# Kernel optimization log

Measured on AMD Instinct MI355X. Metric: run time of the kernel, lower is better.

Reference implementation:

```python
import jax, jax.numpy as jnp
import numpy as np

N = 100000   # n_nodes
E = 800000   # n_edges
IN = 128
HID = 128
OUT = 40
EPS = 1e-5   # BatchNorm1d eps


def setup_inputs() -> dict:
    key = jax.random.key(0)
    ks = jax.random.split(key, 16)
    def w(k, i, o):
        return jax.random.normal(k, (i, o), jnp.float32) / np.sqrt(i).astype(np.float32)
    return {
        "x": jax.random.normal(ks[0], (N, IN), jnp.float32),
        "edge_index": jax.random.randint(ks[1], (2, E), 0, N, dtype=jnp.int64),
        # SAGEConv weights: Wl acts on aggregated neighbors, Wr on root features
        "Wl0": w(ks[2], IN, HID),  "Wr0": w(ks[3], IN, HID),
        "Wl1": w(ks[4], HID, HID), "Wr1": w(ks[5], HID, HID),
        "Wl2": w(ks[6], HID, OUT), "Wr2": w(ks[7], HID, OUT),
        "b2": jnp.zeros((OUT,), jnp.float32),  # bias only on last layer
        # BatchNorm params for layers 0,1 (last layer has no BN)
        "g0": jnp.ones((HID,), jnp.float32), "be0": jnp.zeros((HID,), jnp.float32),
        "g1": jnp.ones((HID,), jnp.float32), "be1": jnp.zeros((HID,), jnp.float32),
    }


def _sage_conv(x, src, dst, Wl, Wr, b=None):
    # mean aggregation of source messages at destination nodes
    msg = x[src]                                             # [E, d] gather
    agg = jax.ops.segment_sum(msg, dst, num_segments=N)      # [N, d]
    cnt = jax.ops.segment_sum(jnp.ones((src.shape[0],), x.dtype), dst,
                              num_segments=N)                # [N]
    mean = agg / jnp.maximum(cnt, 1.0)[:, None]
    out = mean @ Wl + x @ Wr
    if b is not None:
        out = out + b
    return out


def _batch_norm(h, gamma, beta):
    # training-mode BN over node dim, biased variance (matches torch BatchNorm1d)
    mu = h.mean(axis=0)
    var = h.var(axis=0)
    return (h - mu) * jax.lax.rsqrt(var + EPS) * gamma + beta


def reference(x, edge_index, Wl0, Wr0, Wl1, Wr1, Wl2, Wr2, b2, g0, be0, g1, be1):
    src, dst = edge_index[0], edge_index[1]
    h = _sage_conv(x, src, dst, Wl0, Wr0)
    h = jax.nn.relu(_batch_norm(h, g0, be0))
    h = _sage_conv(h, src, dst, Wl1, Wr1)
    h = jax.nn.relu(_batch_norm(h, g1, be1))
    h = _sage_conv(h, src, dst, Wl2, Wr2, b2)
    return h
```

## Files before the change

kernel.cpp:

```cpp
#include <hip/hip_runtime.h>
#include <hip/hip_bf16.h>

#define N_NODES 100000
#define N_EDGES 800000
#define EPS 1e-5f
#define NBANK 32
#define HB_BLOCKS 256
#define HB_PER 3125
#define CS_GPB 64
#define BUCKET_N 12500
#define MROW 68

typedef __attribute__((ext_vector_type(8))) short short8;
typedef __attribute__((ext_vector_type(4))) float floatx4;

__device__ __forceinline__ unsigned short f2b(float f) {
    unsigned int u = __float_as_uint(f);
    u = (u + 0x7fffu + ((u >> 16) & 1u)) >> 16;
    return (unsigned short)u;
}
__device__ __forceinline__ float blo(unsigned int u) { return __uint_as_float(u << 16); }
__device__ __forceinline__ float bhi(unsigned int u) { return __uint_as_float(u & 0xffff0000u); }
__device__ __forceinline__ float b2f(unsigned short s) {
    return __uint_as_float(((unsigned int)s) << 16);
}

__global__ void __launch_bounds__(256) prep_k(const float* __restrict__ x,
                                              unsigned short* __restrict__ o,
                                              const int* __restrict__ dst,
                                              unsigned int* __restrict__ cnt,
                                              unsigned int* __restrict__ bhist) {
    if (blockIdx.x < 12500) {
        int i = blockIdx.x * 256 + threadIdx.x;
        float4 v = ((const float4*)x)[i];
        ushort4 r;
        r.x = f2b(v.x); r.y = f2b(v.y); r.z = f2b(v.z); r.w = f2b(v.w);
        ((ushort4*)o)[i] = r;
        return;
    }
    __shared__ unsigned int lh[8];
    int hb = blockIdx.x - 12500;
    if (threadIdx.x < 8) lh[threadIdx.x] = 0;
    __syncthreads();
    int start = hb * HB_PER;
    for (int i = threadIdx.x; i < HB_PER; i += 256) {
        int d = dst[start + i];
        atomicAdd(&cnt[d], 1u);
        atomicAdd(&lh[(unsigned int)d / BUCKET_N], 1u);
    }
    __syncthreads();
    if (threadIdx.x < 8) bhist[threadIdx.x * HB_BLOCKS + hb] = lh[threadIdx.x];
}

__device__ __forceinline__ void pack_one(const float* __restrict__ Wl,
                                         const float* __restrict__ Wr,
                                         unsigned short* __restrict__ out,
                                         int Hreal, int NCT, int tid) {
    int i = tid & 7;
    int lane = (tid >> 3) & 63;
    int q = tid >> 9;
    int c = q % NCT;
    int t = q / NCT;
    int k = t * 32 + (lane >> 4) * 8 + i;
    int n = c * 16 + (lane & 15);
    float v = 0.f;
    if (n < Hreal) v = (k < 128) ? Wl[k * Hreal + n] : Wr[(k - 128) * Hreal + n];
    out[tid] = f2b(v);
}

__global__ void __launch_bounds__(256) pack_all(const float* __restrict__ Wl0, const float* __restrict__ Wr0,
                                                const float* __restrict__ Wl1, const float* __restrict__ Wr1,
                                                const float* __restrict__ Wl2, const float* __restrict__ Wr2,
                                                unsigned short* __restrict__ W0p,
                                                unsigned short* __restrict__ W1p,
                                                unsigned short* __restrict__ W2p) {
    int tid = blockIdx.x * 256 + threadIdx.x;
    if (tid < 32768) pack_one(Wl0, Wr0, W0p, 128, 8, tid);
    else if (tid < 65536) pack_one(Wl1, Wr1, W1p, 128, 8, tid - 32768);
    else if (tid < 77824) pack_one(Wl2, Wr2, W2p, 40, 3, tid - 65536);
}

__global__ void scan1(const unsigned int* __restrict__ cnt, unsigned int* __restrict__ rowptr,
                      unsigned int* __restrict__ bsum) {
    __shared__ unsigned int sh[256];
    int t = threadIdx.x;
    int i = blockIdx.x * 256 + t;
    unsigned int v = (i < N_NODES) ? cnt[i] : 0u;
    sh[t] = v; __syncthreads();
    for (int off = 1; off < 256; off <<= 1) {
        unsigned int add = (t >= off) ? sh[t - off] : 0u;
        __syncthreads();
        sh[t] += add;
        __syncthreads();
    }
    if (i < N_NODES) rowptr[i] = sh[t] - v;
    if (t == 255) bsum[blockIdx.x] = sh[255];
}

__global__ void scan2_bscan(const unsigned int* __restrict__ bsum, unsigned int* __restrict__ boff,
                            int nb, unsigned int* __restrict__ A) {
    if (blockIdx.x == 0) {
        __shared__ unsigned int sh[512];
        int t = threadIdx.x;
        unsigned int v = (t < nb) ? bsum[t] : 0u;
        sh[t] = v; __syncthreads();
        for (int off = 1; off < 512; off <<= 1) {
            unsigned int add = (t >= off) ? sh[t - off] : 0u;
            __syncthreads();
            sh[t] += add;
            __syncthreads();
        }
        if (t < nb) boff[t] = sh[t] - v;
        return;
    }
    __shared__ unsigned int part[256];
    int t = threadIdx.x;
    unsigned int v[8];
    unsigned int s = 0;
    if (t < 256) {
#pragma unroll
        for (int i = 0; i < 8; i++) { v[i] = A[t * 8 + i]; s += v[i]; }
        part[t] = s;
    }
    __syncthreads();
    for (int off = 1; off < 256; off <<= 1) {
        unsigned int add = (t < 256 && t >= off) ? part[t - off] : 0u;
        __syncthreads();
        if (t < 256) part[t] += add;
        __syncthreads();
    }
    if (t < 256) {
        unsigned int base = part[t] - s;
#pragma unroll
        for (int i = 0; i < 8; i++) { unsigned int old = v[i]; A[t * 8 + i] = base; base += old; }
    }
}

__global__ void __launch_bounds__(256) scan3_bscatter(unsigned int* __restrict__ rowptr,
                                                      const unsigned int* __restrict__ boff,
                                                      unsigned int* __restrict__ cursor,
                                                      const int* __restrict__ src,
                                                      const int* __restrict__ dst,
                                                      const unsigned int* __restrict__ boffs,
                                                      unsigned int* __restrict__ ebuf) {
    if (blockIdx.x < 391) {
        int i = blockIdx.x * 256 + threadIdx.x;
        if (i < N_NODES) {
            unsigned int r = rowptr[i] + boff[blockIdx.x];
            rowptr[i] = r;
            cursor[i] = r;
        }
        if (i == N_NODES) rowptr[N_NODES] = N_EDGES;
        return;
    }
    __shared__ unsigned int cur[8];
    int bb = blockIdx.x - 391;
    if (threadIdx.x < 8) cur[threadIdx.x] = boffs[threadIdx.x * HB_BLOCKS + bb];
    __syncthreads();
    int start = bb * HB_PER;
    for (int i = threadIdx.x; i < HB_PER; i += 256) {
        int d = dst[start + i];
        int s = src[start + i];
        unsigned int b = (unsigned int)d / BUCKET_N;
        unsigned int dl = (unsigned int)d - b * BUCKET_N;
        unsigned int pos = atomicAdd(&cur[b], 1u);
        ebuf[pos] = (unsigned int)s | (dl << 17);
    }
}

__global__ void __launch_bounds__(256) cscatter(const unsigned int* __restrict__ ebuf,
                                                const unsigned int* __restrict__ rowptr,
                                                unsigned int* __restrict__ cursor,
                                                int* __restrict__ srclist) {
    int g = blockIdx.x & 7;
    int gblk = blockIdx.x >> 3;
    unsigned int estart = rowptr[g * BUCKET_N];
    unsigned int eend = (g == 7) ? N_EDGES : rowptr[(g + 1) * BUCKET_N];
    unsigned int nume = eend - estart;
    unsigned int per = (nume + CS_GPB - 1) / CS_GPB;
    unsigned int s0 = estart + gblk * per;
    unsigned int s1 = s0 + per; if (s1 > eend) s1 = eend;
    unsigned int nodebase = g * BUCKET_N;
    for (unsigned int i = s0 + threadIdx.x; i < s1; i += 256) {
        unsigned int p = ebuf[i];
        unsigned int s = p & 0x1FFFFu;
        unsigned int node = nodebase + (p >> 17);
        unsigned int pos = atomicAdd(&cursor[node], 1u);
        srclist[pos] = (int)s;
    }
}

template<int BN>
__device__ __forceinline__ void agg_phase16(const unsigned short* __restrict__ hb,
                                            const unsigned int* __restrict__ rowptr,
                                            const int* __restrict__ srclist,
                                            unsigned int* __restrict__ smean,
                                            const float* __restrict__ sc,
                                            const float* __restrict__ sh,
                                            int wave, int g, int l, int blockrow) {
    const uint4* hp = (const uint4*)hb;
    int nl = wave * 4 + g;
    int node = blockrow + nl;
    float f0 = 0.f, f1 = 0.f, f2 = 0.f, f3 = 0.f, f4 = 0.f, f5 = 0.f, f6 = 0.f, f7 = 0.f;
    float sc0r = 0.f, sc1r = 0.f, sc2r = 0.f, sc3r = 0.f, sc4r = 0.f, sc5r = 0.f, sc6r = 0.f, sc7r = 0.f;
    float sh0r = 0.f, sh1r = 0.f, sh2r = 0.f, sh3r = 0.f, sh4r = 0.f, sh5r = 0.f, sh6r = 0.f, sh7r = 0.f;
    if (BN) {
        const float* s0 = sc + l * 8;
        const float* s1 = sh + l * 8;
        sc0r = s0[0]; sc1r = s0[1]; sc2r = s0[2]; sc3r = s0[3];
        sc4r = s0[4]; sc5r = s0[5]; sc6r = s0[6]; sc7r = s0[7];
        sh0r = s1[0]; sh1r = s1[1]; sh2r = s1[2]; sh3r = s1[3];
        sh4r = s1[4]; sh5r = s1[5]; sh6r = s1[6]; sh7r = s1[7];
    }
    unsigned int b = rowptr[node], e = rowptr[node + 1];
    unsigned int p = b;
#define ACC8(U) { \
    if (BN) { \
        f0 += fmaxf(0.f, fmaf(blo(U.x), sc0r, sh0r)); \
        f1 += fmaxf(0.f, fmaf(bhi(U.x), sc1r, sh1r)); \
        f2 += fmaxf(0.f, fmaf(blo(U.y), sc2r, sh2r)); \
        f3 += fmaxf(0.f, fmaf(bhi(U.y), sc3r, sh3r)); \
        f4 += fmaxf(0.f, fmaf(blo(U.z), sc4r, sh4r)); \
        f5 += fmaxf(0.f, fmaf(bhi(U.z), sc5r, sh5r)); \
        f6 += fmaxf(0.f, fmaf(blo(U.w), sc6r, sh6r)); \
        f7 += fmaxf(0.f, fmaf(bhi(U.w), sc7r, sh7r)); \
    } else { \
        f0 += blo(U.x); f1 += bhi(U.x); f2 += blo(U.y); f3 += bhi(U.y); \
        f4 += blo(U.z); f5 += bhi(U.z); f6 += blo(U.w); f7 += bhi(U.w); \
    } }
    int s0 = 0, s1 = 0, s2 = 0, s3 = 0;
    bool have = (p + 4 <= e);
    if (have) { s0 = srclist[p]; s1 = srclist[p + 1]; s2 = srclist[p + 2]; s3 = srclist[p + 3]; }
    while (have) {
        uint4 u0 = hp[(size_t)s0 * 16 + l];
        uint4 u1 = hp[(size_t)s1 * 16 + l];
        uint4 u2 = hp[(size_t)s2 * 16 + l];
        uint4 u3 = hp[(size_t)s3 * 16 + l];
        p += 4;
        have = (p + 4 <= e);
        if (have) { s0 = srclist[p]; s1 = srclist[p + 1]; s2 = srclist[p + 2]; s3 = srclist[p + 3]; }
        ACC8(u0); ACC8(u1); ACC8(u2); ACC8(u3);
    }
    if (p + 2 <= e) {
        int t0 = srclist[p];
        int t1 = srclist[p + 1];
        uint4 u0 = hp[(size_t)t0 * 16 + l];
        uint4 u1 = hp[(size_t)t1 * 16 + l];
        ACC8(u0); ACC8(u1);
        p += 2;
    }
    if (p < e) {
        int t0 = srclist[p];
        uint4 u0 = hp[(size_t)t0 * 16 + l];
        ACC8(u0);
    }
#undef ACC8
    unsigned int deg = e - b;
    float r = 1.0f / (float)(deg > 1u ? deg : 1u);
    uint4 o;
    o.x = (unsigned int)f2b(f0 * r) | ((unsigned int)f2b(f1 * r) << 16);
    o.y = (unsigned int)f2b(f2 * r) | ((unsigned int)f2b(f3 * r) << 16);
    o.z = (unsigned int)f2b(f4 * r) | ((unsigned int)f2b(f5 * r) << 16);
    o.w = (unsigned int)f2b(f6 * r) | ((unsigned int)f2b(f7 * r) << 16);
    *(uint4*)&smean[nl * MROW + l * 4] = o;
}

__device__ __forceinline__ short8 bn_pack8(short8 raw, const float* __restrict__ scb,
                                           const float* __restrict__ shb, int koff) {
    short8 r;
#pragma unroll
    for (int i = 0; i < 8; i++) {
        float v = b2f((unsigned short)raw[i]);
        v = fmaxf(0.f, fmaf(v, scb[koff + i], shb[koff + i]));
        r[i] = (short)f2b(v);
    }
    return r;
}

template<int BN>
__global__ void __launch_bounds__(256) gemm2f_k(const unsigned short* __restrict__ hb,
                                                const unsigned int* __restrict__ rowptr,
                                                const int* __restrict__ srclist,
                                                const float* __restrict__ sc,
                                                const float* __restrict__ sh,
                                                const unsigned short* __restrict__ Bp,
                                                unsigned short* __restrict__ outb,
                                                float* __restrict__ sums) {
    __shared__ unsigned int smean[16 * MROW];
    __shared__ float lds_s[128];
    __shared__ float lds_s2[128];
    __shared__ float scb[128];
    __shared__ float shb[128];
    int wave = threadIdx.x >> 6;
    int lane = threadIdx.x & 63;
    int quad = lane >> 4;
    int l15 = lane & 15;
    int blockrow = blockIdx.x * 16;

    if (threadIdx.x < 128) {
        lds_s[threadIdx.x] = 0.f; lds_s2[threadIdx.x] = 0.f;
        if (BN) { scb[threadIdx.x] = sc[threadIdx.x]; shb[threadIdx.x] = sh[threadIdx.x]; }
    }
    if (BN) __syncthreads();

    agg_phase16<BN>(hb, rowptr, srclist, smean, sc, sh, wave, quad, l15, blockrow);
    __syncthreads();

    floatx4 acc[2];
    acc[0] = (floatx4){0.f, 0.f, 0.f, 0.f};
    acc[1] = (floatx4){0.f, 0.f, 0.f, 0.f};

    int r0 = blockrow + l15;

#pragma unroll
    for (int t = 0; t < 8; t++) {
        short8 a0;
        if (t < 4) {
            a0 = *(const short8*)&smean[l15 * MROW + t * 16 + quad * 4];
        } else {
            int koff = (t & 3) * 32 + quad * 8;
            short8 raw = *(const short8*)(hb + (size_t)r0 * 128 + koff);
            a0 = BN ? bn_pack8(raw, scb, shb, koff) : raw;
        }
#pragma unroll
        for (int c = 0; c < 2; c++) {
            int cidx = wave * 2 + c;
            short8 bf = *(const short8*)(Bp + ((size_t)(t * 8 + cidx) * 64 + lane) * 8);
            acc[c] = __builtin_amdgcn_mfma_f32_16x16x32_bf16(a0, bf, acc[c], 0, 0, 0);
        }
    }

#pragma unroll
    for (int c = 0; c < 2; c++) {
        int col = wave * 32 + c * 16 + l15;
        float s = 0.f, s2 = 0.f;
#pragma unroll
        for (int r = 0; r < 4; r++) {
            int row = blockrow + quad * 4 + r;
            float v = acc[c][r];
            outb[(size_t)row * 128 + col] = f2b(v);
            s += v; s2 += v * v;
        }
        s += __shfl_xor(s, 16);  s += __shfl_xor(s, 32);
        s2 += __shfl_xor(s2, 16); s2 += __shfl_xor(s2, 32);
        if (quad == 0) {
            atomicAdd(&lds_s[col], s);
            atomicAdd(&lds_s2[col], s2);
        }
    }

    __syncthreads();
    if (threadIdx.x < 128) {
        int bank = blockIdx.x & (NBANK - 1);
        atomicAdd(&sums[bank * 256 + threadIdx.x], lds_s[threadIdx.x]);
        atomicAdd(&sums[bank * 256 + 128 + threadIdx.x], lds_s2[threadIdx.x]);
    }
}

__global__ void __launch_bounds__(192) dense_k(const unsigned short* __restrict__ hb,
                                               const float* __restrict__ sc,
                                               const float* __restrict__ sh,
                                               const unsigned short* __restrict__ Bp,
                                               const float* __restrict__ bias,
                                               unsigned short* __restrict__ P,
                                               float* __restrict__ Q) {
    __shared__ float scb[128];
    __shared__ float shb[128];
    int wave = threadIdx.x >> 6;
    int lane = threadIdx.x & 63;
    int quad = lane >> 4;
    int l15 = lane & 15;
    int blockrow = blockIdx.x * 16;

    if (threadIdx.x < 128) { scb[threadIdx.x] = sc[threadIdx.x]; shb[threadIdx.x] = sh[threadIdx.x]; }
    __syncthreads();

    int r0 = blockrow + l15;
    short8 af[4];
#pragma unroll
    for (int t = 0; t < 4; t++) {
        int koff = t * 32 + quad * 8;
        short8 raw = *(const short8*)(hb + (size_t)r0 * 128 + koff);
        af[t] = bn_pack8(raw, scb, shb, koff);
    }

    floatx4 aP = (floatx4){0.f, 0.f, 0.f, 0.f};
    floatx4 aQ = (floatx4){0.f, 0.f, 0.f, 0.f};
#pragma unroll
    for (int t = 0; t < 4; t++) {
        short8 bl = *(const short8*)(Bp + ((size_t)(t * 3 + wave) * 64 + lane) * 8);
        aP = __builtin_amdgcn_mfma_f32_16x16x32_bf16(af[t], bl, aP, 0, 0, 0);
    }
#pragma unroll
    for (int t = 0; t < 4; t++) {
        short8 br = *(const short8*)(Bp + ((size_t)((t + 4) * 3 + wave) * 64 + lane) * 8);
        aQ = __builtin_amdgcn_mfma_f32_16x16x32_bf16(af[t], br, aQ, 0, 0, 0);
    }
    int col = wave * 16 + l15;
    if (col < 40) {
#pragma unroll
        for (int r = 0; r < 4; r++) {
            int row = blockrow + quad * 4 + r;
            P[(size_t)row * 40 + col] = f2b(aP[r]);
            Q[(size_t)row * 40 + col] = aQ[r] + bias[col];
        }
    }
}

__global__ void __launch_bounds__(256) agg40_k(const unsigned short* __restrict__ P,
                                               const unsigned int* __restrict__ rowptr,
                                               const int* __restrict__ srclist,
                                               const float* __restrict__ Q,
                                               float* __restrict__ out) {
    int tid = threadIdx.x;
    int g = tid >> 3;
    int l = tid & 7;
    int ll = l < 5 ? l : 0;
    int node = blockIdx.x * 32 + g;
    const uint4* pp = (const uint4*)P;
    float f0 = 0.f, f1 = 0.f, f2 = 0.f, f3 = 0.f, f4 = 0.f, f5 = 0.f, f6 = 0.f, f7 = 0.f;
    unsigned int b = rowptr[node], e = rowptr[node + 1];
    unsigned int p = b;
#define ACC8(U) { f0 += blo(U.x); f1 += bhi(U.x); f2 += blo(U.y); f3 += bhi(U.y); \
                  f4 += blo(U.z); f5 += bhi(U.z); f6 += blo(U.w); f7 += bhi(U.w); }
    int s0 = 0, s1 = 0, s2 = 0, s3 = 0;
    bool have = (p + 4 <= e);
    if (have) { s0 = srclist[p]; s1 = srclist[p + 1]; s2 = srclist[p + 2]; s3 = srclist[p + 3]; }
    while (have) {
        uint4 u0 = pp[(size_t)s0 * 5 + ll];
        uint4 u1 = pp[(size_t)s1 * 5 + ll];
        uint4 u2 = pp[(size_t)s2 * 5 + ll];
        uint4 u3 = pp[(size_t)s3 * 5 + ll];
        p += 4;
        have = (p + 4 <= e);
        if (have) { s0 = srclist[p]; s1 = srclist[p + 1]; s2 = srclist[p + 2]; s3 = srclist[p + 3]; }
        ACC8(u0); ACC8(u1); ACC8(u2); ACC8(u3);
    }
    if (p + 2 <= e) {
        int t0 = srclist[p];
        int t1 = srclist[p + 1];
        uint4 u0 = pp[(size_t)t0 * 5 + ll];
        uint4 u1 = pp[(size_t)t1 * 5 + ll];
        ACC8(u0); ACC8(u1);
        p += 2;
    }
    if (p < e) {
        int t0 = srclist[p];
        uint4 u0 = pp[(size_t)t0 * 5 + ll];
        ACC8(u0);
    }
#undef ACC8
    unsigned int deg = e - b;
    float r = 1.0f / (float)(deg > 1u ? deg : 1u);
    if (l < 5) {
        size_t base = (size_t)node * 40 + l * 8;
        float4 o1, o2;
        o1.x = f0 * r + Q[base + 0]; o1.y = f1 * r + Q[base + 1];
        o1.z = f2 * r + Q[base + 2]; o1.w = f3 * r + Q[base + 3];
        o2.x = f4 * r + Q[base + 4]; o2.y = f5 * r + Q[base + 5];
        o2.z = f6 * r + Q[base + 6]; o2.w = f7 * r + Q[base + 7];
        *(float4*)(out + base) = o1;
        *(float4*)(out + base + 4) = o2;
    }
}

__global__ void bn_finalize(const float* __restrict__ sums, const float* __restrict__ g,
                            const float* __restrict__ be, float* __restrict__ sc,
                            float* __restrict__ sh) {
    __shared__ float lds[256];
    int t = threadIdx.x;
    float s = 0.f;
#pragma unroll 8
    for (int bk = 0; bk < NBANK; bk++) s += sums[bk * 256 + t];
    lds[t] = s;
    __syncthreads();
    if (t < 128) {
        float inv_n = 1.0f / (float)N_NODES;
        float mu = lds[t] * inv_n;
        float var = lds[128 + t] * inv_n - mu * mu;
        float sf = g[t] * rsqrtf(var + EPS);
        sc[t] = sf;
        sh[t] = be[t] - mu * sf;
    }
}

extern "C" void kernel_launch(void* const* d_in, const int* in_sizes, int n_in,
                              void* d_out, int out_size, void* d_ws, size_t ws_size,
                              hipStream_t stream) {
    const float* x   = (const float*)d_in[0];
    const int* ei    = (const int*)d_in[1];
    const float* Wl0 = (const float*)d_in[2];
    const float* Wr0 = (const float*)d_in[3];
    const float* Wl1 = (const float*)d_in[4];
    const float* Wr1 = (const float*)d_in[5];
    const float* Wl2 = (const float*)d_in[6];
    const float* Wr2 = (const float*)d_in[7];
    const float* b2  = (const float*)d_in[8];
    const float* g0  = (const float*)d_in[9];
    const float* be0 = (const float*)d_in[10];
    const float* g1  = (const float*)d_in[11];
    const float* be1 = (const float*)d_in[12];

    char* ws = (char*)d_ws;
    size_t off = 0;
    auto alloc = [&](size_t bytes) -> void* {
        void* p = ws + off;
        off += (bytes + 4095) & ~(size_t)4095;
        return p;
    };

    const size_t NB16 = (size_t)N_NODES * 128 * 2;
    unsigned short* xb   = (unsigned short*)alloc(NB16);
    unsigned short* C0b  = (unsigned short*)alloc(NB16);
    unsigned short* C1b  = (unsigned short*)alloc(NB16);
    unsigned int* cnt    = (unsigned int*)alloc((size_t)N_NODES * 4);
    float* sums0         = (float*)alloc(NBANK * 256 * 4);
    float* sums1         = (float*)alloc(NBANK * 256 * 4);
    unsigned int* rowptr = (unsigned int*)alloc((size_t)(N_NODES + 1) * 4);
    unsigned int* cursor = (unsigned int*)alloc((size_t)N_NODES * 4);
    int* srclist         = (int*)alloc((size_t)N_EDGES * 4);
    unsigned int* ebuf   = (unsigned int*)alloc((size_t)N_EDGES * 4);
    unsigned int* bhist  = (unsigned int*)alloc(8 * HB_BLOCKS * 4);
    unsigned int* bsum   = (unsigned int*)alloc(512 * 4);
    unsigned int* boff   = (unsigned int*)alloc(512 * 4);
    float* sc            = (float*)alloc(128 * 4);
    float* sh            = (float*)alloc(128 * 4);
    unsigned short* W0p  = (unsigned short*)alloc(8 * 8 * 64 * 8 * 2);
    unsigned short* W1p  = (unsigned short*)alloc(8 * 8 * 64 * 8 * 2);
    unsigned short* W2p  = (unsigned short*)alloc(3 * 8 * 64 * 8 * 2);

    unsigned short* P40  = C0b;
    float* Q             = (float*)xb;

    const int* srcp = ei;
    const int* dstp = ei + N_EDGES;

    size_t cnt_slab  = ((size_t)N_NODES * 4 + 4095) & ~(size_t)4095;
    size_t sums_slab = ((size_t)NBANK * 256 * 4 + 4095) & ~(size_t)4095;
    hipMemsetAsync(cnt, 0, cnt_slab + 2 * sums_slab, stream);

    prep_k<<<12756, 256, 0, stream>>>(x, xb, dstp, cnt, bhist);
    pack_all<<<304, 256, 0, stream>>>(Wl0, Wr0, Wl1, Wr1, Wl2, Wr2, W0p, W1p, W2p);

    scan1<<<391, 256, 0, stream>>>(cnt, rowptr, bsum);
    scan2_bscan<<<2, 512, 0, stream>>>(bsum, boff, 391, bhist);
    scan3_bscatter<<<647, 256, 0, stream>>>(rowptr, boff, cursor, srcp, dstp, bhist, ebuf);
    cscatter<<<8 * CS_GPB, 256, 0, stream>>>(ebuf, rowptr, cursor, srclist);

    gemm2f_k<0><<<6250, 256, 0, stream>>>(xb, rowptr, srclist, nullptr, nullptr, W0p, C0b, sums0);
    bn_finalize<<<1, 256, 0, stream>>>(sums0, g0, be0, sc, sh);

    gemm2f_k<1><<<6250, 256, 0, stream>>>(C0b, rowptr, srclist, sc, sh, W1p, C1b, sums1);
    bn_finalize<<<1, 256, 0, stream>>>(sums1, g1, be1, sc, sh);

    dense_k<<<6250, 192, 0, stream>>>(C1b, sc, sh, W2p, b2, P40, Q);
    agg40_k<<<3125, 256, 0, stream>>>(P40, rowptr, srclist, Q, (float*)d_out);

    (void)in_sizes; (void)n_in; (void)out_size; (void)ws_size;
}
```

Measured before the change: 360.2 us.

## Replace global-atomic CSR build with per-bucket shared-memory counting sort

Per-node degree counting with global atomics, the three-stage global prefix scan and the global cursor scatter are removed. In their place, one 1024-thread block per destination bucket counts degrees in shared memory, scans them locally, writes rowptr, and scatters source indices with shared-memory atomics. Weight packing is also folded into the prep kernel, and the now-unused count, scan and cursor buffers are dropped, cutting kernel launches and global atomic traffic. The trade-off is that only 8 blocks do the whole sort, each looping over about 100k edges twice, so parallelism in that phase is very low.

```diff
diff --git a/kernel.cpp b/kernel.cpp
--- a/kernel.cpp
+++ b/kernel.cpp
@@ -7,9 +7,10 @@
 #define NBANK 32
 #define HB_BLOCKS 256
 #define HB_PER 3125
-#define CS_GPB 64
 #define BUCKET_N 12500
 #define MROW 68
+#define BST 1024
+#define CPT 13
 
 typedef __attribute__((ext_vector_type(8))) short short8;
 typedef __attribute__((ext_vector_type(4))) float floatx4;
@@ -23,33 +24,6 @@
 __device__ __forceinline__ float bhi(unsigned int u) { return __uint_as_float(u & 0xffff0000u); }
 __device__ __forceinline__ float b2f(unsigned short s) {
     return __uint_as_float(((unsigned int)s) << 16);
-}
-
-__global__ void __launch_bounds__(256) prep_k(const float* __restrict__ x,
-                                              unsigned short* __restrict__ o,
-                                              const int* __restrict__ dst,
-                                              unsigned int* __restrict__ cnt,
-                                              unsigned int* __restrict__ bhist) {
-    if (blockIdx.x < 12500) {
-        int i = blockIdx.x * 256 + threadIdx.x;
-        float4 v = ((const float4*)x)[i];
-        ushort4 r;
-        r.x = f2b(v.x); r.y = f2b(v.y); r.z = f2b(v.z); r.w = f2b(v.w);
-        ((ushort4*)o)[i] = r;
-        return;
-    }
-    __shared__ unsigned int lh[8];
-    int hb = blockIdx.x - 12500;
-    if (threadIdx.x < 8) lh[threadIdx.x] = 0;
-    __syncthreads();
-    int start = hb * HB_PER;
-    for (int i = threadIdx.x; i < HB_PER; i += 256) {
-        int d = dst[start + i];
-        atomicAdd(&cnt[d], 1u);
-        atomicAdd(&lh[(unsigned int)d / BUCKET_N], 1u);
-    }
-    __syncthreads();
-    if (threadIdx.x < 8) bhist[threadIdx.x * HB_BLOCKS + hb] = lh[threadIdx.x];
 }
 
 __device__ __forceinline__ void pack_one(const float* __restrict__ Wl,
@@ -68,96 +42,72 @@
     out[tid] = f2b(v);
 }
 
-__global__ void __launch_bounds__(256) pack_all(const float* __restrict__ Wl0, const float* __restrict__ Wr0,
-                                                const float* __restrict__ Wl1, const float* __restrict__ Wr1,
-                                                const float* __restrict__ Wl2, const float* __restrict__ Wr2,
-                                                unsigned short* __restrict__ W0p,
-                                                unsigned short* __restrict__ W1p,
-                                                unsigned short* __restrict__ W2p) {
-    int tid = blockIdx.x * 256 + threadIdx.x;
+__global__ void __launch_bounds__(256) prep_k(const float* __restrict__ x,
+                                              unsigned short* __restrict__ o,
+                                              const int* __restrict__ dst,
+                                              unsigned int* __restrict__ bhist,
+                                              const float* __restrict__ Wl0, const float* __restrict__ Wr0,
+                                              const float* __restrict__ Wl1, const float* __restrict__ Wr1,
+                                              const float* __restrict__ Wl2, const float* __restrict__ Wr2,
+                                              unsigned short* __restrict__ W0p,
+                                              unsigned short* __restrict__ W1p,
+                                              unsigned short* __restrict__ W2p) {
+    int b = blockIdx.x;
+    if (b < 12500) {
+        int i = b * 256 + threadIdx.x;
+        float4 v = ((const float4*)x)[i];
+        ushort4 r;
+        r.x = f2b(v.x); r.y = f2b(v.y); r.z = f2b(v.z); r.w = f2b(v.w);
+        ((ushort4*)o)[i] = r;
+        return;
+    }
+    if (b < 12756) {
+        __shared__ unsigned int lh[8];
+        int hb = b - 12500;
+        if (threadIdx.x < 8) lh[threadIdx.x] = 0;
+        __syncthreads();
+        int start = hb * HB_PER;
+        for (int i = threadIdx.x; i < HB_PER; i += 256) {
+            int d = dst[start + i];
+            atomicAdd(&lh[(unsigned int)d / BUCKET_N], 1u);
+        }
+        __syncthreads();
+        if (threadIdx.x < 8) bhist[threadIdx.x * HB_BLOCKS + hb] = lh[threadIdx.x];
+        return;
+    }
+    int tid = (b - 12756) * 256 + threadIdx.x;
     if (tid < 32768) pack_one(Wl0, Wr0, W0p, 128, 8, tid);
     else if (tid < 65536) pack_one(Wl1, Wr1, W1p, 128, 8, tid - 32768);
-    else if (tid < 77824) pack_one(Wl2, Wr2, W2p, 40, 3, tid - 65536);
-}
-
-__global__ void scan1(const unsigned int* __restrict__ cnt, unsigned int* __restrict__ rowptr,
-                      unsigned int* __restrict__ bsum) {
-    __shared__ unsigned int sh[256];
-    int t = threadIdx.x;
-    int i = blockIdx.x * 256 + t;
-    unsigned int v = (i < N_NODES) ? cnt[i] : 0u;
-    sh[t] = v; __syncthreads();
-    for (int off = 1; off < 256; off <<= 1) {
-        unsigned int add = (t >= off) ? sh[t - off] : 0u;
-        __syncthreads();
-        sh[t] += add;
-        __syncthreads();
-    }
-    if (i < N_NODES) rowptr[i] = sh[t] - v;
-    if (t == 255) bsum[blockIdx.x] = sh[255];
-}
-
-__global__ void scan2_bscan(const unsigned int* __restrict__ bsum, unsigned int* __restrict__ boff,
-                            int nb, unsigned int* __restrict__ A) {
-    if (blockIdx.x == 0) {
-        __shared__ unsigned int sh[512];
-        int t = threadIdx.x;
-        unsigned int v = (t < nb) ? bsum[t] : 0u;
-        sh[t] = v; __syncthreads();
-        for (int off = 1; off < 512; off <<= 1) {
-            unsigned int add = (t >= off) ? sh[t - off] : 0u;
-            __syncthreads();
-            sh[t] += add;
-            __syncthreads();
-        }
-        if (t < nb) boff[t] = sh[t] - v;
-        return;
-    }
+    else pack_one(Wl2, Wr2, W2p, 40, 3, tid - 65536);
+}
+
+__global__ void bscan(unsigned int* __restrict__ A) {
     __shared__ unsigned int part[256];
     int t = threadIdx.x;
     unsigned int v[8];
     unsigned int s = 0;
-    if (t < 256) {
-#pragma unroll
-        for (int i = 0; i < 8; i++) { v[i] = A[t * 8 + i]; s += v[i]; }
-        part[t] = s;
-    }
-    __syncthreads();
+#pragma unroll
+    for (int i = 0; i < 8; i++) { v[i] = A[t * 8 + i]; s += v[i]; }
+    part[t] = s; __syncthreads();
     for (int off = 1; off < 256; off <<= 1) {
-        unsigned int add = (t < 256 && t >= off) ? part[t - off] : 0u;
+        unsigned int add = (t >= off) ? part[t - off] : 0u;
         __syncthreads();
-        if (t < 256) part[t] += add;
+        part[t] += add;
         __syncthreads();
     }
-    if (t < 256) {
-        unsigned int base = part[t] - s;
-#pragma unroll
-        for (int i = 0; i < 8; i++) { unsigned int old = v[i]; A[t * 8 + i] = base; base += old; }
-    }
-}
-
-__global__ void __launch_bounds__(256) scan3_bscatter(unsigned int* __restrict__ rowptr,
-                                                      const unsigned int* __restrict__ boff,
-                                                      unsigned int* __restrict__ cursor,
-                                                      const int* __restrict__ src,
-                                                      const int* __restrict__ dst,
-                                                      const unsigned int* __restrict__ boffs,
-                                                      unsigned int* __restrict__ ebuf) {
-    if (blockIdx.x < 391) {
-        int i = blockIdx.x * 256 + threadIdx.x;
-        if (i < N_NODES) {
-            unsigned int r = rowptr[i] + boff[blockIdx.x];
-            rowptr[i] = r;
-            cursor[i] = r;
-        }
-        if (i == N_NODES) rowptr[N_NODES] = N_EDGES;
-        return;
-    }
+    unsigned int base = part[t] - s;
+#pragma unroll
+    for (int i = 0; i < 8; i++) { unsigned int old = v[i]; A[t * 8 + i] = base; base += old; }
+}
+
+__global__ void __launch_bounds__(256) bscatter(const int* __restrict__ src,
+                                                const int* __restrict__ dst,
+                                                const unsigned int* __restrict__ boffs,
+                                                unsigned int* __restrict__ ebuf) {
     __shared__ unsigned int cur[8];
-    int bb = blockIdx.x - 391;
-    if (threadIdx.x < 8) cur[threadIdx.x] = boffs[threadIdx.x * HB_BLOCKS + bb];
-    __syncthreads();
-    int start = bb * HB_PER;
+    if (threadIdx.x < 8) cur[threadIdx.x] = boffs[threadIdx.x * HB_BLOCKS + blockIdx.x];
+    __syncthreads();
+    int start = blockIdx.x * HB_PER;
     for (int i = threadIdx.x; i < HB_PER; i += 256) {
         int d = dst[start + i];
         int s = src[start + i];
@@ -168,25 +118,57 @@
     }
 }
 
-__global__ void __launch_bounds__(256) cscatter(const unsigned int* __restrict__ ebuf,
-                                                const unsigned int* __restrict__ rowptr,
-                                                unsigned int* __restrict__ cursor,
-                                                int* __restrict__ srclist) {
-    int g = blockIdx.x & 7;
-    int gblk = blockIdx.x >> 3;
-    unsigned int estart = rowptr[g * BUCKET_N];
-    unsigned int eend = (g == 7) ? N_EDGES : rowptr[(g + 1) * BUCKET_N];
-    unsigned int nume = eend - estart;
-    unsigned int per = (nume + CS_GPB - 1) / CS_GPB;
-    unsigned int s0 = estart + gblk * per;
-    unsigned int s1 = s0 + per; if (s1 > eend) s1 = eend;
-    unsigned int nodebase = g * BUCKET_N;
-    for (unsigned int i = s0 + threadIdx.x; i < s1; i += 256) {
+__global__ void __launch_bounds__(BST) bucket_sort_k(const unsigned int* __restrict__ ebuf,
+                                                     const unsigned int* __restrict__ bhist,
+                                                     unsigned int* __restrict__ rowptr,
+                                                     int* __restrict__ srclist) {
+    __shared__ unsigned int cntl[BUCKET_N];
+    __shared__ unsigned int psum[BST];
+    int g = blockIdx.x;
+    int t = threadIdx.x;
+    unsigned int estart = bhist[g * HB_BLOCKS];
+    unsigned int eend = (g == 7) ? N_EDGES : bhist[(g + 1) * HB_BLOCKS];
+
+    for (int i = t; i < BUCKET_N; i += BST) cntl[i] = 0u;
+    __syncthreads();
+
+    for (unsigned int i = estart + t; i < eend; i += BST)
+        atomicAdd(&cntl[ebuf[i] >> 17], 1u);
+    __syncthreads();
+
+    unsigned int loc[CPT];
+    unsigned int s = 0;
+    int base = t * CPT;
+#pragma unroll
+    for (int i = 0; i < CPT; i++) {
+        unsigned int v = (base + i < BUCKET_N) ? cntl[base + i] : 0u;
+        loc[i] = s;
+        s += v;
+    }
+    psum[t] = s;
+    __syncthreads();
+    for (int off = 1; off < BST; off <<= 1) {
+        unsigned int add = (t >= off) ? psum[t - off] : 0u;
+        __syncthreads();
+        psum[t] += add;
+        __syncthreads();
+    }
+    unsigned int tb = psum[t] - s;
+#pragma unroll
+    for (int i = 0; i < CPT; i++) {
+        if (base + i < BUCKET_N) {
+            unsigned int ol = tb + loc[i];
+            cntl[base + i] = ol;
+            rowptr[g * BUCKET_N + base + i] = estart + ol;
+        }
+    }
+    if (g == 7 && t == 0) rowptr[N_NODES] = N_EDGES;
+    __syncthreads();
+
+    for (unsigned int i = estart + t; i < eend; i += BST) {
         unsigned int p = ebuf[i];
-        unsigned int s = p & 0x1FFFFu;
-        unsigned int node = nodebase + (p >> 17);
-        unsigned int pos = atomicAdd(&cursor[node], 1u);
-        srclist[pos] = (int)s;
+        unsigned int pos = atomicAdd(&cntl[p >> 17], 1u);
+        srclist[estart + pos] = (int)(p & 0x1FFFFu);
     }
 }
 
@@ -513,16 +495,12 @@
     unsigned short* xb   = (unsigned short*)alloc(NB16);
     unsigned short* C0b  = (unsigned short*)alloc(NB16);
     unsigned short* C1b  = (unsigned short*)alloc(NB16);
-    unsigned int* cnt    = (unsigned int*)alloc((size_t)N_NODES * 4);
     float* sums0         = (float*)alloc(NBANK * 256 * 4);
     float* sums1         = (float*)alloc(NBANK * 256 * 4);
     unsigned int* rowptr = (unsigned int*)alloc((size_t)(N_NODES + 1) * 4);
-    unsigned int* cursor = (unsigned int*)alloc((size_t)N_NODES * 4);
     int* srclist         = (int*)alloc((size_t)N_EDGES * 4);
     unsigned int* ebuf   = (unsigned int*)alloc((size_t)N_EDGES * 4);
     unsigned int* bhist  = (unsigned int*)alloc(8 * HB_BLOCKS * 4);
-    unsigned int* bsum   = (unsigned int*)alloc(512 * 4);
-    unsigned int* boff   = (unsigned int*)alloc(512 * 4);
     float* sc            = (float*)alloc(128 * 4);
     float* sh            = (float*)alloc(128 * 4);
     unsigned short* W0p  = (unsigned short*)alloc(8 * 8 * 64 * 8 * 2);
@@ -535,17 +513,14 @@
     const int* srcp = ei;
     const int* dstp = ei + N_EDGES;
 
-    size_t cnt_slab  = ((size_t)N_NODES * 4 + 4095) & ~(size_t)4095;
-    size_t sums_slab = ((size_t)NBANK * 256 * 4 + 4095) & ~(size_t)4095;
-    hipMemsetAsync(cnt, 0, cnt_slab + 2 * sums_slab, stream);
-
-    prep_k<<<12756, 256, 0, stream>>>(x, xb, dstp, cnt, bhist);
-    pack_all<<<304, 256, 0, stream>>>(Wl0, Wr0, Wl1, Wr1, Wl2, Wr2, W0p, W1p, W2p);
-
-    scan1<<<391, 256, 0, stream>>>(cnt, rowptr, bsum);
-    scan2_bscan<<<2, 512, 0, stream>>>(bsum, boff, 391, bhist);
-    scan3_bscatter<<<647, 256, 0, stream>>>(rowptr, boff, cursor, srcp, dstp, bhist, ebuf);
-    cscatter<<<8 * CS_GPB, 256, 0, stream>>>(ebuf, rowptr, cursor, srclist);
+    hipMemsetAsync(sums0, 0, (size_t)2 * NBANK * 256 * 4, stream);
+
+    prep_k<<<13060, 256, 0, stream>>>(x, xb, dstp, bhist,
+                                      Wl0, Wr0, Wl1, Wr1, Wl2, Wr2, W0p, W1p, W2p);
+
+    bscan<<<1, 256, 0, stream>>>(bhist);
+    bscatter<<<HB_BLOCKS, 256, 0, stream>>>(srcp, dstp, bhist, ebuf);
+    bucket_sort_k<<<8, BST, 0, stream>>>(ebuf, bhist, rowptr, srclist);
 
     gemm2f_k<0><<<6250, 256, 0, stream>>>(xb, rowptr, srclist, nullptr, nullptr, W0p, C0b, sums0);
     bn_finalize<<<1, 256, 0, stream>>>(sums0, g0, be0, sc, sh);
```

Result: slower. 375.5 us (+4.3%).
